# Performance work log

Measured on AMD Instinct MI355X. Metric: run time of the kernel, lower is better.

The kernel has to match this reference:

```python
import jax, jax.numpy as jnp
import numpy as np

B, S, D, H = 4, 2048, 768, 12
HD = D // H  # 64
NEG_INF = -1000000000.0


def setup_inputs() -> dict:
    key = jax.random.key(0)
    k1, k2, k3 = jax.random.split(key, 3)
    scale_in = 1.0 / np.sqrt(D)
    return {
        "x": jax.random.normal(k1, (B, S, D), dtype=jnp.float32),
        "W_qkv": jax.random.normal(k2, (D, 3 * D), dtype=jnp.float32) * scale_in,
        "b_qkv": jnp.zeros((3 * D,), dtype=jnp.float32),
        "W_o": jax.random.normal(k3, (D, D), dtype=jnp.float32) * scale_in,
        "b_o": jnp.zeros((D,), dtype=jnp.float32),
    }


def reference(x, W_qkv, b_qkv, W_o, b_o):
    # qkv projection: [B,S,3D]
    qkv = x @ W_qkv + b_qkv
    q, k, v = jnp.split(qkv, 3, axis=-1)
    # split heads -> [B,H,S,HD]
    q = q.reshape(B, S, H, HD).transpose(0, 2, 1, 3)
    k = k.reshape(B, S, H, HD).transpose(0, 2, 1, 3)
    v = v.reshape(B, S, H, HD).transpose(0, 2, 1, 3)
    # scores [B,H,S,S], scaled by sqrt(head_dim)
    attn = jnp.einsum("bhqd,bhkd->bhqk", q, k) / jnp.sqrt(jnp.float32(HD))
    # faithful (idiosyncratic) masking from the original module:
    # attn = attn * mask; attn = attn + NEG_INF * (1 - attn)
    mask = jnp.tril(jnp.ones((S, S), dtype=attn.dtype))  # [S,S]
    attn = attn * mask
    attn = attn + NEG_INF * (1.0 - attn)
    attn = jax.nn.softmax(attn, axis=-1)
    # dropout is identity in inference
    ctx = jnp.einsum("bhqk,bhkd->bhqd", attn, v)  # [B,H,S,HD]
    ctx = ctx.transpose(0, 2, 1, 3).reshape(B, S, D)
    return ctx @ W_o + b_o
```

## Files before the change

### kernel.cpp

```cpp
#include <hip/hip_runtime.h>
#include <cmath>
#include <cstdint>
#include <cstddef>

namespace {
constexpr int kB = 4;
constexpr int kS = 2048;
constexpr int kD = 768;
constexpr int kH = 12;
constexpr int kHD = 64;
constexpr int k3D = 3 * kD;
constexpr float kNeg = -1000000000.0f;
constexpr float kDelta = 0.25f;
constexpr int kNQK = 1536;

constexpr size_t kOfsQkv = 0;
constexpr size_t kOfsCtx = (size_t)kB * kS * k3D * 4;
constexpr size_t kOfsXh  = kOfsCtx + (size_t)kB * kS * kD * 4;
constexpr size_t kSzX    = (size_t)kB * kS * kD * 2;
constexpr size_t kOfsWh  = kOfsXh + 3 * kSzX;
constexpr size_t kSzW    = (size_t)kD * kNQK * 2;
constexpr size_t kNeedWs = kOfsWh + 3 * kSzW;
}

__device__ __forceinline__ float mask_affine(float a) {
#pragma clang fp contract(off)
    const float u = 1.0f - a;
    return a + kNeg * u;
}

__device__ __forceinline__ short bf16rne_s(float f) {
    uint32_t u = __builtin_bit_cast(uint32_t, f);
    u += 0x7FFFu + ((u >> 16) & 1u);
    return (short)(u >> 16);
}
__device__ __forceinline__ float bf16tof(short h) {
    const uint32_t u = ((uint32_t)(unsigned short)h) << 16;
    return __builtin_bit_cast(float, u);
}
__device__ __forceinline__ void split3(float v, unsigned short& h,
                                       unsigned short& m, unsigned short& l) {
    const short hs = bf16rne_s(v);
    const float r1 = v - bf16tof(hs);
    const short ms = bf16rne_s(r1);
    const float r2 = r1 - bf16tof(ms);
    h = (unsigned short)hs;
    m = (unsigned short)ms;
    l = (unsigned short)bf16rne_s(r2);
}

template <int BM, int BN, int BK, int TM, int TN>
__global__ __launch_bounds__(BM * BN / (TM * TN))
void gemm_bias_kernel(const float* __restrict__ A, const float* __restrict__ Bm,
                      const float* __restrict__ bias, float* __restrict__ C,
                      int M, int K, int ldb, int ldc)
{
    constexpr int THREADS = BM * BN / (TM * TN);
    constexpr int TX = BN / TN;
    constexpr int TY = THREADS / TX;
    static_assert(TX == 16 && TY * TM == BM, "geometry");
    constexpr int AF4 = BM * BK / (THREADS * 4);
    constexpr int BF4 = BK * BN / (THREADS * 4);
    constexpr int BSTR = BK * TN + 4;

    __shared__ float As[2][BK][BM + 4];
    __shared__ float Bs[2][TX][BSTR];

    const int tid = threadIdx.x;
    const int tx = tid % TX, ty = tid / TX;
    const int m0 = blockIdx.y * BM, n0 = blockIdx.x * BN;

    float4 pa[AF4], pb[BF4];
    auto load_tiles = [&](int k0) {
#pragma unroll
        for (int it = 0; it < AF4; ++it) {
            const int e = (tid + it * THREADS) * 4;
            const int row = e / BK, col = e % BK;
            pa[it] = *reinterpret_cast<const float4*>(
                &A[(size_t)(m0 + row) * K + (k0 + col)]);
        }
#pragma unroll
        for (int it = 0; it < BF4; ++it) {
            const int e = (tid + it * THREADS) * 4;
            const int row = e / BN, col = e % BN;
            pb[it] = *reinterpret_cast<const float4*>(
                &Bm[(size_t)(k0 + row) * ldb + (n0 + col)]);
        }
    };
    auto commit = [&](int buf) {
#pragma unroll
        for (int it = 0; it < AF4; ++it) {
            const int e = (tid + it * THREADS) * 4;
            const int row = e / BK, col = e % BK;
            As[buf][col + 0][row] = pa[it].x;
            As[buf][col + 1][row] = pa[it].y;
            As[buf][col + 2][row] = pa[it].z;
            As[buf][col + 3][row] = pa[it].w;
        }
#pragma unroll
        for (int it = 0; it < BF4; ++it) {
            const int e = (tid + it * THREADS) * 4;
            const int row = e / BN, col = e % BN;
            const int g = col / TN, off = col % TN;
            *reinterpret_cast<float4*>(&Bs[buf][g][row * TN + off]) = pb[it];
        }
    };

    float acc[TM][TN];
#pragma unroll
    for (int i = 0; i < TM; ++i)
#pragma unroll
        for (int j = 0; j < TN; ++j) acc[i][j] = 0.0f;

    load_tiles(0);
    commit(0);
    load_tiles(BK);
    __syncthreads();

    int cur = 0;
    for (int k0 = 0; k0 < K; k0 += BK) {
        const bool has_next = (k0 + BK < K);
        if (has_next) {
            commit(cur ^ 1);
            if (k0 + 2 * BK < K) load_tiles(k0 + 2 * BK);
        }
#pragma unroll
        for (int kk = 0; kk < BK; ++kk) {
            float a[TM], b[TN];
#pragma unroll
            for (int i = 0; i < TM; i += 4) {
                const float4 v = *reinterpret_cast<const float4*>(
                    &As[cur][kk][ty * TM + i]);
                a[i] = v.x; a[i + 1] = v.y; a[i + 2] = v.z; a[i + 3] = v.w;
            }
#pragma unroll
            for (int j = 0; j < TN; j += 4) {
                const float4 v = *reinterpret_cast<const float4*>(
                    &Bs[cur][tx][kk * TN + j]);
                b[j] = v.x; b[j + 1] = v.y; b[j + 2] = v.z; b[j + 3] = v.w;
            }
#pragma unroll
            for (int i = 0; i < TM; ++i)
#pragma unroll
                for (int j = 0; j < TN; ++j)
                    acc[i][j] = fmaf(a[i], b[j], acc[i][j]);
        }
        if (has_next) __syncthreads();
        cur ^= 1;
    }

#pragma unroll
    for (int i = 0; i < TM; ++i) {
        const int m = m0 + ty * TM + i;
#pragma unroll
        for (int j = 0; j < TN; ++j) {
            const int n = n0 + tx * TN + j;
            C[(size_t)m * ldc + n] = acc[i][j] + bias[n];
        }
    }
}

__global__ __launch_bounds__(256)
void split_x_kernel(const float* __restrict__ x, unsigned short* __restrict__ xh,
                    unsigned short* __restrict__ xm, unsigned short* __restrict__ xl)
{
    const size_t total4 = (size_t)kB * kS * kD / 4;
    for (size_t i4 = blockIdx.x * 256 + threadIdx.x; i4 < total4;
         i4 += (size_t)gridDim.x * 256) {
        const float4 v = *reinterpret_cast<const float4*>(&x[i4 * 4]);
        ushort4 h, m, l;
        split3(v.x, h.x, m.x, l.x);
        split3(v.y, h.y, m.y, l.y);
        split3(v.z, h.z, m.z, l.z);
        split3(v.w, h.w, m.w, l.w);
        *reinterpret_cast<ushort4*>(&xh[i4 * 4]) = h;
        *reinterpret_cast<ushort4*>(&xm[i4 * 4]) = m;
        *reinterpret_cast<ushort4*>(&xl[i4 * 4]) = l;
    }
}

__global__ __launch_bounds__(256)
void split_w_kernel(const float* __restrict__ W,
                    unsigned short* __restrict__ Wh,
                    unsigned short* __restrict__ Wm,
                    unsigned short* __restrict__ Wl)
{
    __shared__ unsigned short Th[64][72], Tm[64][72], Tl[64][72];
    const int k0 = blockIdx.x * 64, n0 = blockIdx.y * 64;
    const int tid = threadIdx.x;

#pragma unroll
    for (int i = 0; i < 16; ++i) {
        const int idx = tid + i * 256;
        const int kk = idx >> 6, nn = idx & 63;
        const float v = W[(size_t)(k0 + kk) * k3D + (n0 + nn)];
        split3(v, Th[nn][kk], Tm[nn][kk], Tl[nn][kk]);
    }
    __syncthreads();
#pragma unroll
    for (int i = 0; i < 16; ++i) {
        const int idx = tid + i * 256;
        const int nn = idx >> 6, kk = idx & 63;
        const size_t o = (size_t)(n0 + nn) * kD + (k0 + kk);
        Wh[o] = Th[nn][kk];
        Wm[o] = Tm[nn][kk];
        Wl[o] = Tl[nn][kk];
    }
}

__global__ __launch_bounds__(256)
void qk_mfma_kernel(const unsigned short* __restrict__ xh,
                    const unsigned short* __restrict__ xm,
                    const unsigned short* __restrict__ xl,
                    const unsigned short* __restrict__ Wh,
                    const unsigned short* __restrict__ Wm,
                    const unsigned short* __restrict__ Wl,
                    const float* __restrict__ bias, float* __restrict__ C)
{
    using f32x4 = __attribute__((ext_vector_type(4))) float;
    using s16x8 = __attribute__((ext_vector_type(8))) short;

    __shared__ unsigned short Axs[3][128][40];
    __shared__ unsigned short Bxs[3][64][40];

    const int tid = threadIdx.x;
    const int wave = tid >> 6, lane = tid & 63;
    const int jq = lane & 15, hi = lane >> 4;
    const int n0 = blockIdx.x * 64, m0 = blockIdx.y * 128;

    const unsigned short* Xs[3] = {xh, xm, xl};
    const unsigned short* Ws[3] = {Wh, Wm, Wl};

    f32x4 acc[2][4];
#pragma unroll
    for (int i = 0; i < 2; ++i)
#pragma unroll
        for (int j = 0; j < 4; ++j) acc[i][j] = {0.f, 0.f, 0.f, 0.f};

    for (int kt = 0; kt < kD / 32; ++kt) {
        const int k0 = kt * 32;
        __syncthreads();
#pragma unroll
        for (int s = 0; s < 3; ++s) {
#pragma unroll
            for (int it = 0; it < 4; ++it) {
                const int e = (tid + it * 256) * 4;
                const int row = e >> 5, col = e & 31;
                *reinterpret_cast<ushort4*>(&Axs[s][row][col]) =
                    *reinterpret_cast<const ushort4*>(
                        &Xs[s][(size_t)(m0 + row) * kD + (k0 + col)]);
            }
#pragma unroll
            for (int it = 0; it < 2; ++it) {
                const int e = (tid + it * 256) * 4;
                const int row = e >> 5, col = e & 31;
                *reinterpret_cast<ushort4*>(&Bxs[s][row][col]) =
                    *reinterpret_cast<const ushort4*>(
                        &Ws[s][(size_t)(n0 + row) * kD + (k0 + col)]);
            }
        }
        __syncthreads();

        s16x8 af[2][3];
#pragma unroll
        for (int i = 0; i < 2; ++i)
#pragma unroll
            for (int s = 0; s < 3; ++s)
                af[i][s] = *reinterpret_cast<const s16x8*>(
                    &Axs[s][wave * 32 + i * 16 + jq][hi * 8]);

#pragma unroll
        for (int j = 0; j < 4; ++j) {
            s16x8 bf[3];
#pragma unroll
            for (int s = 0; s < 3; ++s)
                bf[s] = *reinterpret_cast<const s16x8*>(
                    &Bxs[s][j * 16 + jq][hi * 8]);
#pragma unroll
            for (int i = 0; i < 2; ++i) {
                f32x4 c = acc[i][j];
                c = __builtin_amdgcn_mfma_f32_16x16x32_bf16(af[i][0], bf[0], c, 0, 0, 0);
                c = __builtin_amdgcn_mfma_f32_16x16x32_bf16(af[i][1], bf[0], c, 0, 0, 0);
                c = __builtin_amdgcn_mfma_f32_16x16x32_bf16(af[i][0], bf[1], c, 0, 0, 0);
                c = __builtin_amdgcn_mfma_f32_16x16x32_bf16(af[i][2], bf[0], c, 0, 0, 0);
                c = __builtin_amdgcn_mfma_f32_16x16x32_bf16(af[i][1], bf[1], c, 0, 0, 0);
                c = __builtin_amdgcn_mfma_f32_16x16x32_bf16(af[i][0], bf[2], c, 0, 0, 0);
                c = __builtin_amdgcn_mfma_f32_16x16x32_bf16(af[i][2], bf[1], c, 0, 0, 0);
                c = __builtin_amdgcn_mfma_f32_16x16x32_bf16(af[i][1], bf[2], c, 0, 0, 0);
                acc[i][j] = c;
            }
        }
    }

#pragma unroll
    for (int i = 0; i < 2; ++i) {
        const int mbase = m0 + wave * 32 + i * 16 + hi * 4;
#pragma unroll
        for (int j = 0; j < 4; ++j) {
            const int n = n0 + j * 16 + jq;
            const float bv = bias[n];
#pragma unroll
            for (int r = 0; r < 4; ++r)
                C[(size_t)(mbase + r) * k3D + n] = acc[i][j][r] + bv;
        }
    }
}

__global__ __launch_bounds__(256)
void gemm_mfma_kernel(const float* __restrict__ A, const float* __restrict__ Bm,
                      const float* __restrict__ bias, float* __restrict__ C,
                      int M, int K, int ldb, int ldc)
{
    using f32x4 = __attribute__((ext_vector_type(4))) float;
    using s16x8 = __attribute__((ext_vector_type(8))) short;
    constexpr int BM = 128, BN = 64, BK = 32;
    constexpr int AST = 40;

    __shared__ unsigned short Ah[2][BM][AST];
    __shared__ unsigned short Al[2][BM][AST];
    __shared__ unsigned short Bh[2][BN][AST];

    const int tid = threadIdx.x;
    const int wave = tid >> 6, lane = tid & 63;
    const int jq = lane & 15, hi = lane >> 4;
    const int m0 = blockIdx.y * BM, n0 = blockIdx.x * BN;

    float4 pa[4], pb[2];
    auto load_tiles = [&](int k0) {
#pragma unroll
        for (int it = 0; it < 4; ++it) {
            const int e = (tid + it * 256) * 4;
            const int row = e / BK, col = e % BK;
            pa[it] = *reinterpret_cast<const float4*>(
                &A[(size_t)(m0 + row) * K + (k0 + col)]);
        }
#pragma unroll
        for (int it = 0; it < 2; ++it) {
            const int e = (tid + it * 256) * 4;
            const int krow = e / BN, ncol = e % BN;
            pb[it] = *reinterpret_cast<const float4*>(
                &Bm[(size_t)(k0 + krow) * ldb + (n0 + ncol)]);
        }
    };
    auto commit = [&](int buf) {
#pragma unroll
        for (int it = 0; it < 4; ++it) {
            const int e = (tid + it * 256) * 4;
            const int row = e / BK, col = e % BK;
            const float v[4] = {pa[it].x, pa[it].y, pa[it].z, pa[it].w};
            ushort4 uh, ul;
            unsigned short* ph = &uh.x;
            unsigned short* pl = &ul.x;
#pragma unroll
            for (int r = 0; r < 4; ++r) {
                const short hb = bf16rne_s(v[r]);
                ph[r] = (unsigned short)hb;
                pl[r] = (unsigned short)bf16rne_s(v[r] - bf16tof(hb));
            }
            *reinterpret_cast<ushort4*>(&Ah[buf][row][col]) = uh;
            *reinterpret_cast<ushort4*>(&Al[buf][row][col]) = ul;
        }
#pragma unroll
        for (int it = 0; it < 2; ++it) {
            const int e = (tid + it * 256) * 4;
            const int krow = e / BN, ncol = e % BN;
            Bh[buf][ncol + 0][krow] = (unsigned short)bf16rne_s(pb[it].x);
            Bh[buf][ncol + 1][krow] = (unsigned short)bf16rne_s(pb[it].y);
            Bh[buf][ncol + 2][krow] = (unsigned short)bf16rne_s(pb[it].z);
            Bh[buf][ncol + 3][krow] = (unsigned short)bf16rne_s(pb[it].w);
        }
    };

    f32x4 acc[2][4];
#pragma unroll
    for (int i = 0; i < 2; ++i)
#pragma unroll
        for (int j = 0; j < 4; ++j) acc[i][j] = {0.f, 0.f, 0.f, 0.f};

    load_tiles(0);
    commit(0);
    load_tiles(BK);
    __syncthreads();

    int cur = 0;
    for (int k0 = 0; k0 < K; k0 += BK) {
        const bool has_next = (k0 + BK < K);
        if (has_next) {
            commit(cur ^ 1);
            if (k0 + 2 * BK < K) load_tiles(k0 + 2 * BK);
        }
        s16x8 ahf[2], alf[2], bhf[4];
#pragma unroll
        for (int i = 0; i < 2; ++i) {
            ahf[i] = *reinterpret_cast<const s16x8*>(
                &Ah[cur][wave * 32 + i * 16 + jq][hi * 8]);
            alf[i] = *reinterpret_cast<const s16x8*>(
                &Al[cur][wave * 32 + i * 16 + jq][hi * 8]);
        }
#pragma unroll
        for (int j = 0; j < 4; ++j)
            bhf[j] = *reinterpret_cast<const s16x8*>(
                &Bh[cur][j * 16 + jq][hi * 8]);
#pragma unroll
        for (int i = 0; i < 2; ++i)
#pragma unroll
            for (int j = 0; j < 4; ++j) {
                f32x4 c = acc[i][j];
                c = __builtin_amdgcn_mfma_f32_16x16x32_bf16(ahf[i], bhf[j], c, 0, 0, 0);
                c = __builtin_amdgcn_mfma_f32_16x16x32_bf16(alf[i], bhf[j], c, 0, 0, 0);
                acc[i][j] = c;
            }
        if (has_next) __syncthreads();
        cur ^= 1;
    }

#pragma unroll
    for (int i = 0; i < 2; ++i) {
        const int mbase = m0 + wave * 32 + i * 16 + hi * 4;
#pragma unroll
        for (int j = 0; j < 4; ++j) {
            const int n = n0 + j * 16 + jq;
            const float bv = bias[n];
#pragma unroll
            for (int r = 0; r < 4; ++r)
                C[(size_t)(mbase + r) * ldc + n] = acc[i][j][r] + bv;
        }
    }
}

__global__ __launch_bounds__(256)
void vsuf_kernel(const float* __restrict__ qkv, float* __restrict__ vsuf)
{
    const int h = blockIdx.x, b = blockIdx.y;
    const int lane = threadIdx.x & 63, wave = threadIdx.x >> 6;
    const float* vp = qkv + (size_t)b * kS * k3D + 2 * kD + h * kHD;
    float* op = vsuf + (size_t)(b * kH + h) * kS * kHD;
    __shared__ float csum[4][64];

    const int kBeg = wave * 512, kEnd = kBeg + 512;
    float s = 0.0f;
#pragma unroll 8
    for (int k = kBeg; k < kEnd; ++k)
        s += vp[(size_t)k * k3D + lane];
    csum[wave][lane] = s;
    __syncthreads();

    float run = 0.0f;
    for (int w = wave + 1; w < 4; ++w) run += csum[w][lane];
#pragma unroll 8
    for (int k = kEnd - 1; k >= kBeg; --k) {
        run += vp[(size_t)k * k3D + lane];
        op[(size_t)k * kHD + lane] = run;
    }
}

__global__ __launch_bounds__(256, 3)
void attn_mfma_kernel(const float* __restrict__ qkv,
                      const float* __restrict__ vsuf,
                      float* __restrict__ ctx)
{
    using f32x4 = __attribute__((ext_vector_type(4))) float;
    using s16x8 = __attribute__((ext_vector_type(8))) short;

    const int id = blockIdx.x;
    const int bh = id % (kB * kH);
    const int t  = id / (kB * kH);
    const int b = bh / kH, h = bh % kH;

    const int tid = threadIdx.x;
    const int wave = tid >> 6, lane = tid & 63;
    const int jq = lane & 15, hi = lane >> 4;
    const int qrow = wave * 16 + jq;
    const int qglob = t * 64 + qrow;

    __shared__ float Qf[64][68];
    __shared__ float Kf[64][68];
    __shared__ unsigned short Kb[64][72];
    __shared__ float Msh[64];
    __shared__ float MgS[64];
    __shared__ int   CgS[64], I0S[64], I1S[64];

    const float* qp = qkv + (size_t)b * kS * k3D + h * kHD;
    const float* kp = qp + kD;
    const float* vp = qp + 2 * kD;

#pragma unroll
    for (int i = 0; i < 4; ++i) {
        const int f4 = tid + i * 256;
        const int r = f4 >> 4, d4 = f4 & 15;
        float4 v = *reinterpret_cast<const float4*>(
            &qp[(size_t)(t * 64 + r) * k3D + d4 * 4]);
        v.x *= 0.125f; v.y *= 0.125f; v.z *= 0.125f; v.w *= 0.125f;
        *reinterpret_cast<float4*>(&Qf[r][d4 * 4]) = v;
    }
    __syncthreads();

    auto mkfrag = [&](const float* p) {
        const float4 a = *reinterpret_cast<const float4*>(p);
        const float4 c = *reinterpret_cast<const float4*>(p + 4);
        s16x8 r;
        r[0] = bf16rne_s(a.x); r[1] = bf16rne_s(a.y);
        r[2] = bf16rne_s(a.z); r[3] = bf16rne_s(a.w);
        r[4] = bf16rne_s(c.x); r[5] = bf16rne_s(c.y);
        r[6] = bf16rne_s(c.z); r[7] = bf16rne_s(c.w);
        return r;
    };

    const s16x8 bq0 = mkfrag(&Qf[qrow][hi * 8]);
    const s16x8 bq1 = mkfrag(&Qf[qrow][32 + hi * 8]);

    auto stage_kb = [&](int kt) {
#pragma unroll
        for (int i = 0; i < 4; ++i) {
            const int f4 = tid + i * 256;
            const int r = f4 >> 4, d4 = f4 & 15;
            const float4 v = *reinterpret_cast<const float4*>(
                &kp[(size_t)(kt * 64 + r) * k3D + d4 * 4]);
            ushort4 u;
            u.x = (unsigned short)bf16rne_s(v.x);
            u.y = (unsigned short)bf16rne_s(v.y);
            u.z = (unsigned short)bf16rne_s(v.z);
            u.w = (unsigned short)bf16rne_s(v.w);
            *reinterpret_cast<ushort4*>(&Kb[r][d4 * 4]) = u;
        }
    };
    auto stage_both = [&](int kt) {
#pragma unroll
        for (int i = 0; i < 4; ++i) {
            const int f4 = tid + i * 256;
            const int r = f4 >> 4, d4 = f4 & 15;
            const float4 v = *reinterpret_cast<const float4*>(
                &kp[(size_t)(kt * 64 + r) * k3D + d4 * 4]);
            *reinterpret_cast<float4*>(&Kf[r][d4 * 4]) = v;
            ushort4 u;
            u.x = (unsigned short)bf16rne_s(v.x);
            u.y = (unsigned short)bf16rne_s(v.y);
            u.z = (unsigned short)bf16rne_s(v.z);
            u.w = (unsigned short)bf16rne_s(v.w);
            *reinterpret_cast<ushort4*>(&Kb[r][d4 * 4]) = u;
        }
    };

    auto score_tile = [&](f32x4* acc) {
#pragma unroll
        for (int g = 0; g < 4; ++g) {
            const s16x8 a0 = *reinterpret_cast<const s16x8*>(
                &Kb[g * 16 + jq][hi * 8]);
            const s16x8 a1 = *reinterpret_cast<const s16x8*>(
                &Kb[g * 16 + jq][32 + hi * 8]);
            f32x4 c = {0.f, 0.f, 0.f, 0.f};
            c = __builtin_amdgcn_mfma_f32_16x16x32_bf16(a0, bq0, c, 0, 0, 0);
            c = __builtin_amdgcn_mfma_f32_16x16x32_bf16(a1, bq1, c, 0, 0, 0);
            acc[g] = c;
        }
    };

    float mt = -INFINITY;
    for (int kt = 0; kt <= t; ++kt) {
        __syncthreads();
        stage_kb(kt);
        __syncthreads();
        f32x4 acc[4];
        score_tile(acc);
#pragma unroll
        for (int g = 0; g < 4; ++g)
#pragma unroll
            for (int r = 0; r < 4; ++r) {
                const int key = kt * 64 + g * 16 + hi * 4 + r;
                if (key <= qglob) mt = fmaxf(mt, acc[g][r]);
            }
    }
    mt = fmaxf(mt, __shfl_xor(mt, 16));
    mt = fmaxf(mt, __shfl_xor(mt, 32));
    if (hi == 0) Msh[wave * 16 + jq] = mt;
    __syncthreads();
    const float thr = Msh[wave * 16 + jq] - kDelta;

    float m = -INFINITY;
    int cnt = 0, i0 = -1, i1 = -1;
    for (int kt = 0; kt <= t; ++kt) {
        __syncthreads();
        stage_both(kt);
        __syncthreads();
        f32x4 acc[4];
        score_tile(acc);
#pragma unroll
        for (int g = 0; g < 4; ++g)
#pragma unroll
            for (int r = 0; r < 4; ++r) {
                const int key = kt * 64 + g * 16 + hi * 4 + r;
                if (key <= qglob && acc[g][r] > thr) {
                    const float* qr = &Qf[qrow][0];
                    const float* kr = &Kf[key - kt * 64][0];
                    float dot = 0.0f;
#pragma unroll
                    for (int d4 = 0; d4 < 16; ++d4) {
                        const float4 q4 = *reinterpret_cast<const float4*>(qr + d4 * 4);
                        const float4 k4 = *reinterpret_cast<const float4*>(kr + d4 * 4);
                        dot = fmaf(q4.x, k4.x, dot);
                        dot = fmaf(q4.y, k4.y, dot);
                        dot = fmaf(q4.z, k4.z, dot);
                        dot = fmaf(q4.w, k4.w, dot);
                    }
                    const float s = mask_affine(dot);
                    const bool upd = (s > m), tie = (s == m);
                    i1 = upd ? -1 : ((tie && cnt == 1) ? key : i1);
                    i0 = upd ? key : i0;
                    cnt = upd ? 1 : (tie ? cnt + 1 : cnt);
                    m = upd ? s : m;
                }
            }
    }

#pragma unroll
    for (int off = 16; off <= 32; off <<= 1) {
        const float mo = __shfl_xor(m, off);
        const int co = __shfl_xor(cnt, off);
        const int o0 = __shfl_xor(i0, off);
        const int o1 = __shfl_xor(i1, off);
        if (mo > m) { m = mo; cnt = co; i0 = o0; i1 = o1; }
        else if (mo == m && co > 0) {
            if (cnt == 0) { i0 = o0; i1 = o1; }
            else if (cnt == 1) { i1 = o0; }
            cnt += co;
        }
    }
    if (hi == 0) {
        MgS[wave * 16 + jq] = m; CgS[wave * 16 + jq] = cnt;
        I0S[wave * 16 + jq] = i0; I1S[wave * 16 + jq] = i1;
    }
    __syncthreads();

    const int qloc = tid >> 2, qtr = tid & 3;
    const int qi = t * 64 + qloc;
    float mg = MgS[qloc];
    int fcnt = CgS[qloc], f0 = I0S[qloc], f1 = I1S[qloc];

    bool addsuf = false;
    if (qi < kS - 1) {
        const bool lt = (mg < kNeg), eq = (mg == kNeg);
        if (lt)      { fcnt = kS - 1 - qi; f0 = -1; f1 = -1; addsuf = true; }
        else if (eq) { fcnt += kS - 1 - qi; addsuf = true; }
    }

    float4 a4[4];
#pragma unroll
    for (int i = 0; i < 4; ++i) a4[i] = {0.f, 0.f, 0.f, 0.f};

    if (f0 >= 0) {
        const float* vr = vp + (size_t)f0 * k3D + qtr * 16;
#pragma unroll
        for (int i = 0; i < 4; ++i) {
            const float4 v = *reinterpret_cast<const float4*>(vr + i * 4);
            a4[i].x += v.x; a4[i].y += v.y; a4[i].z += v.z; a4[i].w += v.w;
        }
    }
    if (f1 >= 0) {
        const float* vr = vp + (size_t)f1 * k3D + qtr * 16;
#pragma unroll
        for (int i = 0; i < 4; ++i) {
            const float4 v = *reinterpret_cast<const float4*>(vr + i * 4);
            a4[i].x += v.x; a4[i].y += v.y; a4[i].z += v.z; a4[i].w += v.w;
        }
    }
    if (addsuf) {
        const float* sp = vsuf + ((size_t)(b * kH + h) * kS + (qi + 1)) * kHD
                          + qtr * 16;
#pragma unroll
        for (int i = 0; i < 4; ++i) {
            const float4 v = *reinterpret_cast<const float4*>(sp + i * 4);
            a4[i].x += v.x; a4[i].y += v.y; a4[i].z += v.z; a4[i].w += v.w;
        }
    }

    float* op = ctx + ((size_t)b * kS + qi) * kD + h * kHD + qtr * 16;
    const float fc = (float)fcnt;
#pragma unroll
    for (int i = 0; i < 4; ++i) {
        const float4 r = {a4[i].x / fc, a4[i].y / fc, a4[i].z / fc, a4[i].w / fc};
        *reinterpret_cast<float4*>(op + i * 4) = r;
    }
}

extern "C" void kernel_launch(void* const* d_in, const int* in_sizes, int n_in,
                              void* d_out, int out_size, void* d_ws, size_t ws_size,
                              hipStream_t stream)
{
    const float* x     = (const float*)d_in[0];
    const float* W_qkv = (const float*)d_in[1];
    const float* b_qkv = (const float*)d_in[2];
    const float* W_o   = (const float*)d_in[3];
    const float* b_o   = (const float*)d_in[4];
    float* out = (float*)d_out;

    char* ws = (char*)d_ws;
    float* qkv  = (float*)(ws + kOfsQkv);
    float* ctx  = (float*)(ws + kOfsCtx);
    float* vsuf = out;

    if (ws_size >= kNeedWs) {
        unsigned short* xh = (unsigned short*)(ws + kOfsXh);
        unsigned short* xm = xh + (size_t)kB * kS * kD;
        unsigned short* xl = xm + (size_t)kB * kS * kD;
        unsigned short* Wh = (unsigned short*)(ws + kOfsWh);
        unsigned short* Wm = Wh + (size_t)kD * kNQK;
        unsigned short* Wl = Wm + (size_t)kD * kNQK;

        split_x_kernel<<<dim3(1024), 256, 0, stream>>>(x, xh, xm, xl);
        split_w_kernel<<<dim3(kD / 64, kNQK / 64), 256, 0, stream>>>(
            W_qkv, Wh, Wm, Wl);
        qk_mfma_kernel<<<dim3(kNQK / 64, (kB * kS) / 128), 256, 0, stream>>>(
            xh, xm, xl, Wh, Wm, Wl, b_qkv, qkv);
    } else {
        dim3 grid(kNQK / 128, (kB * kS) / 128);
        gemm_bias_kernel<128, 128, 16, 8, 8><<<grid, 256, 0, stream>>>(
            x, W_qkv, b_qkv, qkv, kB * kS, kD, k3D, k3D);
    }
    {
        dim3 grid(kD / 64, (kB * kS) / 128);
        gemm_mfma_kernel<<<grid, 256, 0, stream>>>(
            x, W_qkv + 2 * kD, b_qkv + 2 * kD, qkv + 2 * kD,
            kB * kS, kD, k3D, k3D);
    }
    {
        dim3 grid(kH, kB);
        vsuf_kernel<<<grid, 256, 0, stream>>>(qkv, vsuf);
    }
    {
        attn_mfma_kernel<<<dim3((kS / 64) * kB * kH), 256, 0, stream>>>(
            qkv, vsuf, ctx);
    }
    {
        dim3 grid(kD / 64, (kB * kS) / 128);
        gemm_mfma_kernel<<<grid, 256, 0, stream>>>(
            ctx, W_o, b_o, out, kB * kS, kD, kD, kD);
    }
}
```

Baseline: 476.5 us.

## Precompute bf16 K once and run barrier-free per-wave attention scan with register double-buffering

Adds a kernel that converts K to a compact bf16 buffer once per head, instead of reconverting it in every query-tile block. The attention kernel is restructured so each wave independently handles two 16-query groups. K fragments are read straight from global memory into double-buffered registers, with no shared memory or __syncthreads. Tiles are ordered longest-first to balance the causal workload. The exact fp32 rescoring now reads Q and K rows from global memory rather than LDS, and the output is written one row per lane-loop, which may cost extra global traffic.

```diff
diff --git a/kernel.cpp b/kernel.cpp
--- a/kernel.cpp
+++ b/kernel.cpp
@@ -21,6 +21,7 @@
 constexpr size_t kOfsWh  = kOfsXh + 3 * kSzX;
 constexpr size_t kSzW    = (size_t)kD * kNQK * 2;
 constexpr size_t kNeedWs = kOfsWh + 3 * kSzW;
+constexpr size_t kOfsKb  = kOfsXh;
 }
 
 __device__ __forceinline__ float mask_affine(float a) {
@@ -454,231 +455,203 @@
     }
 }
 
+__global__ __launch_bounds__(256)
+void conv_k_kernel(const float* __restrict__ qkv, unsigned short* __restrict__ kb)
+{
+    const int h = blockIdx.x, b = blockIdx.y;
+    const float* kp = qkv + (size_t)b * kS * k3D + kD + h * kHD;
+    unsigned short* ob = kb + (size_t)(b * kH + h) * kS * kHD;
+    for (int i = threadIdx.x; i < kS * 16; i += 256) {
+        const int s = i >> 4, d4 = i & 15;
+        const float4 v = *reinterpret_cast<const float4*>(
+            &kp[(size_t)s * k3D + d4 * 4]);
+        ushort4 u;
+        u.x = (unsigned short)bf16rne_s(v.x);
+        u.y = (unsigned short)bf16rne_s(v.y);
+        u.z = (unsigned short)bf16rne_s(v.z);
+        u.w = (unsigned short)bf16rne_s(v.w);
+        *reinterpret_cast<ushort4*>(&ob[s * kHD + d4 * 4]) = u;
+    }
+}
+
 __global__ __launch_bounds__(256, 3)
-void attn_mfma_kernel(const float* __restrict__ qkv,
+void attn_scan_kernel(const float* __restrict__ qkv,
+                      const unsigned short* __restrict__ kb,
                       const float* __restrict__ vsuf,
                       float* __restrict__ ctx)
 {
     using f32x4 = __attribute__((ext_vector_type(4))) float;
     using s16x8 = __attribute__((ext_vector_type(8))) short;
 
-    const int id = blockIdx.x;
-    const int bh = id % (kB * kH);
-    const int t  = id / (kB * kH);
+    const int gw = blockIdx.x * 4 + (threadIdx.x >> 6);
+    const int lane = threadIdx.x & 63;
+    const int jq = lane & 15, hi = lane >> 4;
+    const int p = gw >> 1, half = gw & 1;
+    const int bh = p % (kB * kH);
+    const int t = (kS / 64 - 1) - (p / (kB * kH));
     const int b = bh / kH, h = bh % kH;
-
-    const int tid = threadIdx.x;
-    const int wave = tid >> 6, lane = tid & 63;
-    const int jq = lane & 15, hi = lane >> 4;
-    const int qrow = wave * 16 + jq;
-    const int qglob = t * 64 + qrow;
-
-    __shared__ float Qf[64][68];
-    __shared__ float Kf[64][68];
-    __shared__ unsigned short Kb[64][72];
-    __shared__ float Msh[64];
-    __shared__ float MgS[64];
-    __shared__ int   CgS[64], I0S[64], I1S[64];
 
     const float* qp = qkv + (size_t)b * kS * k3D + h * kHD;
     const float* kp = qp + kD;
     const float* vp = qp + 2 * kD;
-
-#pragma unroll
-    for (int i = 0; i < 4; ++i) {
-        const int f4 = tid + i * 256;
-        const int r = f4 >> 4, d4 = f4 & 15;
-        float4 v = *reinterpret_cast<const float4*>(
-            &qp[(size_t)(t * 64 + r) * k3D + d4 * 4]);
-        v.x *= 0.125f; v.y *= 0.125f; v.z *= 0.125f; v.w *= 0.125f;
-        *reinterpret_cast<float4*>(&Qf[r][d4 * 4]) = v;
-    }
-    __syncthreads();
-
-    auto mkfrag = [&](const float* p) {
-        const float4 a = *reinterpret_cast<const float4*>(p);
-        const float4 c = *reinterpret_cast<const float4*>(p + 4);
-        s16x8 r;
-        r[0] = bf16rne_s(a.x); r[1] = bf16rne_s(a.y);
-        r[2] = bf16rne_s(a.z); r[3] = bf16rne_s(a.w);
-        r[4] = bf16rne_s(c.x); r[5] = bf16rne_s(c.y);
-        r[6] = bf16rne_s(c.z); r[7] = bf16rne_s(c.w);
-        return r;
+    const unsigned short* kbh = kb + (size_t)bh * kS * kHD;
+
+    int qrow[2];
+    s16x8 bq[2][2];
+#pragma unroll
+    for (int q2 = 0; q2 < 2; ++q2) {
+        qrow[q2] = t * 64 + (half * 2 + q2) * 16 + jq;
+        const float* qr = qp + (size_t)qrow[q2] * k3D;
+#pragma unroll
+        for (int fhalf = 0; fhalf < 2; ++fhalf) {
+            const float* pp = qr + fhalf * 32 + hi * 8;
+            const float4 a = *reinterpret_cast<const float4*>(pp);
+            const float4 c = *reinterpret_cast<const float4*>(pp + 4);
+            s16x8 r;
+            r[0] = bf16rne_s(a.x * 0.125f); r[1] = bf16rne_s(a.y * 0.125f);
+            r[2] = bf16rne_s(a.z * 0.125f); r[3] = bf16rne_s(a.w * 0.125f);
+            r[4] = bf16rne_s(c.x * 0.125f); r[5] = bf16rne_s(c.y * 0.125f);
+            r[6] = bf16rne_s(c.z * 0.125f); r[7] = bf16rne_s(c.w * 0.125f);
+            bq[q2][fhalf] = r;
+        }
+    }
+
+    auto load_frags = [&](int kt, s16x8* f) {
+#pragma unroll
+        for (int g = 0; g < 4; ++g) {
+            const unsigned short* base =
+                kbh + (size_t)(kt * 64 + g * 16 + jq) * kHD + hi * 8;
+            f[g * 2 + 0] = *reinterpret_cast<const s16x8*>(base);
+            f[g * 2 + 1] = *reinterpret_cast<const s16x8*>(base + 32);
+        }
     };
 
-    const s16x8 bq0 = mkfrag(&Qf[qrow][hi * 8]);
-    const s16x8 bq1 = mkfrag(&Qf[qrow][32 + hi * 8]);
-
-    auto stage_kb = [&](int kt) {
-#pragma unroll
-        for (int i = 0; i < 4; ++i) {
-            const int f4 = tid + i * 256;
-            const int r = f4 >> 4, d4 = f4 & 15;
-            const float4 v = *reinterpret_cast<const float4*>(
-                &kp[(size_t)(kt * 64 + r) * k3D + d4 * 4]);
-            ushort4 u;
-            u.x = (unsigned short)bf16rne_s(v.x);
-            u.y = (unsigned short)bf16rne_s(v.y);
-            u.z = (unsigned short)bf16rne_s(v.z);
-            u.w = (unsigned short)bf16rne_s(v.w);
-            *reinterpret_cast<ushort4*>(&Kb[r][d4 * 4]) = u;
-        }
+    const int n = t + 1;
+    s16x8 fA[8], fB[8];
+
+    float mt[2] = {-INFINITY, -INFINITY};
+    auto scan1 = [&](int kt, const s16x8* f) {
+#pragma unroll
+        for (int g = 0; g < 4; ++g)
+#pragma unroll
+            for (int q2 = 0; q2 < 2; ++q2) {
+                f32x4 c = {0.f, 0.f, 0.f, 0.f};
+                c = __builtin_amdgcn_mfma_f32_16x16x32_bf16(f[g * 2], bq[q2][0], c, 0, 0, 0);
+                c = __builtin_amdgcn_mfma_f32_16x16x32_bf16(f[g * 2 + 1], bq[q2][1], c, 0, 0, 0);
+#pragma unroll
+                for (int r = 0; r < 4; ++r) {
+                    const int key = kt * 64 + g * 16 + hi * 4 + r;
+                    if (key <= qrow[q2]) mt[q2] = fmaxf(mt[q2], c[r]);
+                }
+            }
     };
-    auto stage_both = [&](int kt) {
-#pragma unroll
-        for (int i = 0; i < 4; ++i) {
-            const int f4 = tid + i * 256;
-            const int r = f4 >> 4, d4 = f4 & 15;
-            const float4 v = *reinterpret_cast<const float4*>(
-                &kp[(size_t)(kt * 64 + r) * k3D + d4 * 4]);
-            *reinterpret_cast<float4*>(&Kf[r][d4 * 4]) = v;
-            ushort4 u;
-            u.x = (unsigned short)bf16rne_s(v.x);
-            u.y = (unsigned short)bf16rne_s(v.y);
-            u.z = (unsigned short)bf16rne_s(v.z);
-            u.w = (unsigned short)bf16rne_s(v.w);
-            *reinterpret_cast<ushort4*>(&Kb[r][d4 * 4]) = u;
-        }
+    load_frags(0, fA);
+    for (int kt = 0; kt < n; ++kt) {
+        if ((kt & 1) == 0) {
+            if (kt + 1 < n) load_frags(kt + 1, fB);
+            scan1(kt, fA);
+        } else {
+            if (kt + 1 < n) load_frags(kt + 1, fA);
+            scan1(kt, fB);
+        }
+    }
+    float thr[2];
+#pragma unroll
+    for (int q2 = 0; q2 < 2; ++q2) {
+        float v = mt[q2];
+        v = fmaxf(v, __shfl_xor(v, 16));
+        v = fmaxf(v, __shfl_xor(v, 32));
+        thr[q2] = v - kDelta;
+    }
+
+    float m[2] = {-INFINITY, -INFINITY};
+    int cnt[2] = {0, 0}, i0[2] = {-1, -1}, i1[2] = {-1, -1};
+    auto scan2 = [&](int kt, const s16x8* f) {
+#pragma unroll
+        for (int g = 0; g < 4; ++g)
+#pragma unroll
+            for (int q2 = 0; q2 < 2; ++q2) {
+                f32x4 c = {0.f, 0.f, 0.f, 0.f};
+                c = __builtin_amdgcn_mfma_f32_16x16x32_bf16(f[g * 2], bq[q2][0], c, 0, 0, 0);
+                c = __builtin_amdgcn_mfma_f32_16x16x32_bf16(f[g * 2 + 1], bq[q2][1], c, 0, 0, 0);
+#pragma unroll
+                for (int r = 0; r < 4; ++r) {
+                    const int key = kt * 64 + g * 16 + hi * 4 + r;
+                    if (key <= qrow[q2] && c[r] > thr[q2]) {
+                        const float* qr = qp + (size_t)qrow[q2] * k3D;
+                        const float* kr = kp + (size_t)key * k3D;
+                        float dot = 0.0f;
+#pragma unroll
+                        for (int d4 = 0; d4 < 16; ++d4) {
+                            const float4 q4 = *reinterpret_cast<const float4*>(qr + d4 * 4);
+                            const float4 k4 = *reinterpret_cast<const float4*>(kr + d4 * 4);
+                            dot = fmaf(q4.x * 0.125f, k4.x, dot);
+                            dot = fmaf(q4.y * 0.125f, k4.y, dot);
+                            dot = fmaf(q4.z * 0.125f, k4.z, dot);
+                            dot = fmaf(q4.w * 0.125f, k4.w, dot);
+                        }
+                        const float s = mask_affine(dot);
+                        const bool upd = (s > m[q2]), tie = (s == m[q2]);
+                        i1[q2] = upd ? -1 : ((tie && cnt[q2] == 1) ? key : i1[q2]);
+                        i0[q2] = upd ? key : i0[q2];
+                        cnt[q2] = upd ? 1 : (tie ? cnt[q2] + 1 : cnt[q2]);
+                        m[q2] = upd ? s : m[q2];
+                    }
+                }
+            }
     };
-
-    auto score_tile = [&](f32x4* acc) {
-#pragma unroll
-        for (int g = 0; g < 4; ++g) {
-            const s16x8 a0 = *reinterpret_cast<const s16x8*>(
-                &Kb[g * 16 + jq][hi * 8]);
-            const s16x8 a1 = *reinterpret_cast<const s16x8*>(
-                &Kb[g * 16 + jq][32 + hi * 8]);
-            f32x4 c = {0.f, 0.f, 0.f, 0.f};
-            c = __builtin_amdgcn_mfma_f32_16x16x32_bf16(a0, bq0, c, 0, 0, 0);
-            c = __builtin_amdgcn_mfma_f32_16x16x32_bf16(a1, bq1, c, 0, 0, 0);
-            acc[g] = c;
-        }
-    };
-
-    float mt = -INFINITY;
-    for (int kt = 0; kt <= t; ++kt) {
-        __syncthreads();
-        stage_kb(kt);
-        __syncthreads();
-        f32x4 acc[4];
-        score_tile(acc);
-#pragma unroll
-        for (int g = 0; g < 4; ++g)
-#pragma unroll
-            for (int r = 0; r < 4; ++r) {
-                const int key = kt * 64 + g * 16 + hi * 4 + r;
-                if (key <= qglob) mt = fmaxf(mt, acc[g][r]);
-            }
-    }
-    mt = fmaxf(mt, __shfl_xor(mt, 16));
-    mt = fmaxf(mt, __shfl_xor(mt, 32));
-    if (hi == 0) Msh[wave * 16 + jq] = mt;
-    __syncthreads();
-    const float thr = Msh[wave * 16 + jq] - kDelta;
-
-    float m = -INFINITY;
-    int cnt = 0, i0 = -1, i1 = -1;
-    for (int kt = 0; kt <= t; ++kt) {
-        __syncthreads();
-        stage_both(kt);
-        __syncthreads();
-        f32x4 acc[4];
-        score_tile(acc);
-#pragma unroll
-        for (int g = 0; g < 4; ++g)
-#pragma unroll
-            for (int r = 0; r < 4; ++r) {
-                const int key = kt * 64 + g * 16 + hi * 4 + r;
-                if (key <= qglob && acc[g][r] > thr) {
-                    const float* qr = &Qf[qrow][0];
-                    const float* kr = &Kf[key - kt * 64][0];
-                    float dot = 0.0f;
-#pragma unroll
-                    for (int d4 = 0; d4 < 16; ++d4) {
-                        const float4 q4 = *reinterpret_cast<const float4*>(qr + d4 * 4);
-                        const float4 k4 = *reinterpret_cast<const float4*>(kr + d4 * 4);
-                        dot = fmaf(q4.x, k4.x, dot);
-                        dot = fmaf(q4.y, k4.y, dot);
-                        dot = fmaf(q4.z, k4.z, dot);
-                        dot = fmaf(q4.w, k4.w, dot);
-                    }
-                    const float s = mask_affine(dot);
-                    const bool upd = (s > m), tie = (s == m);
-                    i1 = upd ? -1 : ((tie && cnt == 1) ? key : i1);
-                    i0 = upd ? key : i0;
-                    cnt = upd ? 1 : (tie ? cnt + 1 : cnt);
-                    m = upd ? s : m;
-                }
-            }
-    }
-
-#pragma unroll
-    for (int off = 16; off <= 32; off <<= 1) {
-        const float mo = __shfl_xor(m, off);
-        const int co = __shfl_xor(cnt, off);
-        const int o0 = __shfl_xor(i0, off);
-        const int o1 = __shfl_xor(i1, off);
-        if (mo > m) { m = mo; cnt = co; i0 = o0; i1 = o1; }
-        else if (mo == m && co > 0) {
-            if (cnt == 0) { i0 = o0; i1 = o1; }
-            else if (cnt == 1) { i1 = o0; }
-            cnt += co;
-        }
-    }
-    if (hi == 0) {
-        MgS[wave * 16 + jq] = m; CgS[wave * 16 + jq] = cnt;
-        I0S[wave * 16 + jq] = i0; I1S[wave * 16 + jq] = i1;
-    }
-    __syncthreads();
-
-    const int qloc = tid >> 2, qtr = tid & 3;
-    const int qi = t * 64 + qloc;
-    float mg = MgS[qloc];
-    int fcnt = CgS[qloc], f0 = I0S[qloc], f1 = I1S[qloc];
-
-    bool addsuf = false;
-    if (qi < kS - 1) {
-        const bool lt = (mg < kNeg), eq = (mg == kNeg);
-        if (lt)      { fcnt = kS - 1 - qi; f0 = -1; f1 = -1; addsuf = true; }
-        else if (eq) { fcnt += kS - 1 - qi; addsuf = true; }
-    }
-
-    float4 a4[4];
-#pragma unroll
-    for (int i = 0; i < 4; ++i) a4[i] = {0.f, 0.f, 0.f, 0.f};
-
-    if (f0 >= 0) {
-        const float* vr = vp + (size_t)f0 * k3D + qtr * 16;
-#pragma unroll
-        for (int i = 0; i < 4; ++i) {
-            const float4 v = *reinterpret_cast<const float4*>(vr + i * 4);
-            a4[i].x += v.x; a4[i].y += v.y; a4[i].z += v.z; a4[i].w += v.w;
-        }
-    }
-    if (f1 >= 0) {
-        const float* vr = vp + (size_t)f1 * k3D + qtr * 16;
-#pragma unroll
-        for (int i = 0; i < 4; ++i) {
-            const float4 v = *reinterpret_cast<const float4*>(vr + i * 4);
-            a4[i].x += v.x; a4[i].y += v.y; a4[i].z += v.z; a4[i].w += v.w;
-        }
-    }
-    if (addsuf) {
-        const float* sp = vsuf + ((size_t)(b * kH + h) * kS + (qi + 1)) * kHD
-                          + qtr * 16;
-#pragma unroll
-        for (int i = 0; i < 4; ++i) {
-            const float4 v = *reinterpret_cast<const float4*>(sp + i * 4);
-            a4[i].x += v.x; a4[i].y += v.y; a4[i].z += v.z; a4[i].w += v.w;
-        }
-    }
-
-    float* op = ctx + ((size_t)b * kS + qi) * kD + h * kHD + qtr * 16;
-    const float fc = (float)fcnt;
-#pragma unroll
-    for (int i = 0; i < 4; ++i) {
-        const float4 r = {a4[i].x / fc, a4[i].y / fc, a4[i].z / fc, a4[i].w / fc};
-        *reinterpret_cast<float4*>(op + i * 4) = r;
+    load_frags(0, fA);
+    for (int kt = 0; kt < n; ++kt) {
+        if ((kt & 1) == 0) {
+            if (kt + 1 < n) load_frags(kt + 1, fB);
+            scan2(kt, fA);
+        } else {
+            if (kt + 1 < n) load_frags(kt + 1, fA);
+            scan2(kt, fB);
+        }
+    }
+
+#pragma unroll
+    for (int q2 = 0; q2 < 2; ++q2) {
+#pragma unroll
+        for (int off = 16; off <= 32; off <<= 1) {
+            const float mo = __shfl_xor(m[q2], off);
+            const int co = __shfl_xor(cnt[q2], off);
+            const int o0 = __shfl_xor(i0[q2], off);
+            const int o1 = __shfl_xor(i1[q2], off);
+            if (mo > m[q2]) { m[q2] = mo; cnt[q2] = co; i0[q2] = o0; i1[q2] = o1; }
+            else if (mo == m[q2] && co > 0) {
+                if (cnt[q2] == 0) { i0[q2] = o0; i1[q2] = o1; }
+                else if (cnt[q2] == 1) { i1[q2] = o0; }
+                cnt[q2] += co;
+            }
+        }
+    }
+
+#pragma unroll
+    for (int q2 = 0; q2 < 2; ++q2) {
+        for (int jj = 0; jj < 16; ++jj) {
+            const float mg = __shfl(m[q2], jj);
+            int fcnt = __shfl(cnt[q2], jj);
+            int f0 = __shfl(i0[q2], jj);
+            int f1 = __shfl(i1[q2], jj);
+            const int qi = t * 64 + (half * 2 + q2) * 16 + jj;
+
+            bool addsuf = false;
+            if (qi < kS - 1) {
+                const bool lt = (mg < kNeg), eq = (mg == kNeg);
+                if (lt)      { fcnt = kS - 1 - qi; f0 = -1; f1 = -1; addsuf = true; }
+                else if (eq) { fcnt += kS - 1 - qi; addsuf = true; }
+            }
+
+            float acc = 0.0f;
+            if (f0 >= 0) acc += vp[(size_t)f0 * k3D + lane];
+            if (f1 >= 0) acc += vp[(size_t)f1 * k3D + lane];
+            if (addsuf)
+                acc += vsuf[((size_t)bh * kS + qi + 1) * kHD + lane];
+
+            ctx[((size_t)b * kS + qi) * kD + h * kHD + lane] = acc / (float)fcnt;
+        }
     }
 }
 
@@ -697,6 +670,7 @@
     float* qkv  = (float*)(ws + kOfsQkv);
     float* ctx  = (float*)(ws + kOfsCtx);
     float* vsuf = out;
+    unsigned short* kbp = (unsigned short*)(ws + kOfsKb);
 
     if (ws_size >= kNeedWs) {
         unsigned short* xh = (unsigned short*)(ws + kOfsXh);
@@ -725,10 +699,11 @@
     {
         dim3 grid(kH, kB);
         vsuf_kernel<<<grid, 256, 0, stream>>>(qkv, vsuf);
+        conv_k_kernel<<<grid, 256, 0, stream>>>(qkv, kbp);
     }
     {
-        attn_mfma_kernel<<<dim3((kS / 64) * kB * kH), 256, 0, stream>>>(
-            qkv, vsuf, ctx);
+        attn_scan_kernel<<<dim3((kB * kH) * (kS / 64) * 2 / 4), 256, 0, stream>>>(
+            qkv, kbp, vsuf, ctx);
     }
     {
         dim3 grid(kD / 64, (kB * kS) / 128);
```

Measured after the change: 1.651 ms. 3.46x slower.
